# Kernel optimization log

Hardware: AMD Instinct MI355X
Metric: run time of the kernel (lower is better)

Reference implementation:

```python
import jax, jax.numpy as jnp
import numpy as np

SCORE_THRESH = 0.25
NMS_THRESH = 0.45
DETECTIONS = 100   # self.detections
K_CAND = 300       # fixed pre-NMS candidate count (jit-friendly stand-in for torch.where filtering)
STRIDES = (8, 16, 32)


def setup_inputs() -> dict:
    key = jax.random.key(0)
    ks = jax.random.split(key, 5)
    pred_p3 = jax.random.normal(ks[0], (16, 80, 80, 3, 85), jnp.float32)
    pred_p4 = jax.random.normal(ks[1], (16, 40, 40, 3, 85), jnp.float32)
    pred_p5 = jax.random.normal(ks[2], (16, 20, 20, 3, 85), jnp.float32)
    anchors = jnp.array([[[10, 13], [16, 30], [33, 23]],
                         [[30, 61], [62, 45], [59, 119]],
                         [[116, 90], [156, 198], [373, 326]]], jnp.float32)
    image_shapes = jnp.full((16, 2), 640, jnp.int32)  # (h, w) per image
    scale_factors = jax.random.uniform(ks[3], (16,), jnp.float32, 0.5, 1.5)
    return {"pred_p3": pred_p3, "pred_p4": pred_p4, "pred_p5": pred_p5,
            "anchors": anchors, "image_shapes": image_shapes,
            "scale_factors": scale_factors, "max_size": 4096}


def _decode_level(p, stride, anchor_wh):
    # p: [B,H,W,A,5+C] already sigmoided
    B, H, W, A, _ = p.shape
    gx = jnp.arange(W, dtype=p.dtype)
    gy = jnp.arange(H, dtype=p.dtype)
    grid = jnp.stack(jnp.meshgrid(gx, gy, indexing='xy'), axis=-1)  # [H,W,2] = (x,y)
    xy = (2.0 * p[..., :2] - 0.5 + grid[None, :, :, None, :]) * stride
    wh = 4.0 * p[..., 2:4] ** 2 * anchor_wh  # anchor_wh: [A,2]
    box = jnp.concatenate([xy, wh], axis=-1).reshape(B, H * W * A, 4)
    obj = p[..., 4].reshape(B, H * W * A)
    cls = p[..., 5:].reshape(B, H * W * A, -1)
    return box, obj, cls


def _pairwise_iou(b):  # b: [K,4] xyxy
    area = (b[:, 2] - b[:, 0]) * (b[:, 3] - b[:, 1])
    lt = jnp.maximum(b[:, None, :2], b[None, :, :2])
    rb = jnp.minimum(b[:, None, 2:], b[None, :, 2:])
    wh = jnp.clip(rb - lt, 0.0)
    inter = wh[..., 0] * wh[..., 1]
    return inter / (area[:, None] + area[None, :] - inter + 1e-9)


def _nms_image(boxes, scores, labels, im_shape, scale, max_size):
    # boxes [K,4], scores [K] sorted desc, labels [K] int
    w = im_shape[1].astype(boxes.dtype)
    h = im_shape[0].astype(boxes.dtype)
    boxes = jnp.stack([jnp.clip(boxes[:, 0], 0.0, w), jnp.clip(boxes[:, 1], 0.0, h),
                       jnp.clip(boxes[:, 2], 0.0, w), jnp.clip(boxes[:, 3], 0.0, h)], axis=1)
    # class-offset boxes (batched_nms)
    bn = jax.lax.stop_gradient(boxes + (labels.astype(boxes.dtype) * max_size)[:, None])
    iou = _pairwise_iou(bn)
    s_ng = jax.lax.stop_gradient(scores)
    K = boxes.shape[0]
    ar = jnp.arange(K)

    def body(i, keep):
        active = keep[i] & (s_ng[i] > SCORE_THRESH)
        return keep & ~((iou[i] > NMS_THRESH) & (ar > i) & active)

    keep = jax.lax.fori_loop(0, K, body, jnp.ones(K, bool))
    final = jnp.where(keep & (s_ng > SCORE_THRESH), scores, 0.0)
    det_s, det_i = jax.lax.top_k(final, DETECTIONS)
    det_b = boxes[det_i] / scale
    det_l = labels[det_i].astype(boxes.dtype)
    return jnp.concatenate([det_b, det_s[:, None], det_l[:, None]], axis=1)  # [D,6]


def reference(pred_p3, pred_p4, pred_p5, anchors, image_shapes, scale_factors, max_size):
    boxes_l, obj_l, cls_l = [], [], []
    for i, (pred, stride) in enumerate(zip((pred_p3, pred_p4, pred_p5), STRIDES)):
        p = jax.nn.sigmoid(pred)
        b, o, c = _decode_level(p, float(stride), anchors[i])
        boxes_l.append(b); obj_l.append(o); cls_l.append(c)
    boxes = jnp.concatenate(boxes_l, axis=1)   # [B,N,4] cxcywh
    obj = jnp.concatenate(obj_l, axis=1)       # [B,N]
    cls = jnp.concatenate(cls_l, axis=1)       # [B,N,C]
    # cxcywh -> xyxy
    cx, cy, ww, hh = boxes[..., 0], boxes[..., 1], boxes[..., 2], boxes[..., 3]
    boxes = jnp.stack([cx - ww / 2, cy - hh / 2, cx + ww / 2, cy + hh / 2], axis=-1)
    B, N, C = cls.shape
    logits = obj[..., None] * cls              # [B,N,C]
    valid = (obj[..., None] > SCORE_THRESH) & (logits > SCORE_THRESH)
    flat = jnp.where(valid, logits, 0.0).reshape(B, N * C)
    vals, idx = jax.lax.top_k(flat, K_CAND)    # sorted desc per image
    aidx = idx // C
    labels = idx % C
    cand_boxes = jnp.take_along_axis(boxes, aidx[..., None], axis=1)  # [B,K,4]
    out = jax.vmap(_nms_image, in_axes=(0, 0, 0, 0, 0, None))(
        cand_boxes, vals, labels, image_shapes, scale_factors, jnp.float32(max_size))
    return out  # [B, DETECTIONS, 6] = (x1,y1,x2,y2,score,label)
```

## Files before the change

kernel.cpp:

```cpp
#include <hip/hip_runtime.h>
#include <cstdint>
#include <cstddef>

#define BATCH 16
#define NCLS 80
#define NANCH 25200
#define ABINS 512
#define SBINS 1024
#define SCAP 2048
#define SCAP2 4096
#define LCAP 1024
#define KC 300
#define DET 100
#define SCORE_T 0.25f
#define NMS_T 0.45f
#define NBLK 50
#define SPAN 504
#define CNTPAD 16

#define TILES_PER_IMG 1575
#define TOT_TILES (BATCH * TILES_PER_IMG)
#define KMAX_BLOCKS 1575

__device__ __forceinline__ float sg(float x) { return 1.0f / (1.0f + expf(-x)); }

__device__ __forceinline__ const float* anchor_base(const float* p3, const float* p4,
                                                    const float* p5, int b, int n) {
    if (n < 19200) return p3 + ((size_t)b * 19200 + n) * 85;
    if (n < 24000) return p4 + ((size_t)b * 4800 + (n - 19200)) * 85;
    return p5 + ((size_t)b * 1200 + (n - 24000)) * 85;
}

__global__ __launch_bounds__(256) void k_max(const float* __restrict__ p3,
                                             const float* __restrict__ p4,
                                             const float* __restrict__ p5,
                                             float* __restrict__ gmax,
                                             unsigned int* __restrict__ ahist) {
    __shared__ __align__(16) float4 wbuf[4][340];
    int tid = threadIdx.x;
    int lane = tid & 63, wv = tid >> 6;
    float4* slot = wbuf[wv];
    const float* sf = (const float*)slot;
    int wid = blockIdx.x * 4 + wv;
    int g = lane >> 2, r = lane & 3;

    for (int t = wid; t < TOT_TILES; t += KMAX_BLOCKS * 4) {
        int b = t / TILES_PER_IMG, lt = t % TILES_PER_IMG;
        const float* src; int gidx;
        if (lt < 1200)      { src = p3 + ((size_t)b * 19200 + lt * 16) * 85;          gidx = lt * 16; }
        else if (lt < 1500) { src = p4 + ((size_t)b * 4800 + (lt - 1200) * 16) * 85;  gidx = 19200 + (lt - 1200) * 16; }
        else                { src = p5 + ((size_t)b * 1200 + (lt - 1500) * 16) * 85;  gidx = 24000 + (lt - 1500) * 16; }
        const float4* tp = (const float4*)src;

        float4 v0 = tp[lane];
        float4 v1 = tp[lane + 64];
        float4 v2 = tp[lane + 128];
        float4 v3 = tp[lane + 192];
        float4 v4 = tp[lane + 256];
        float4 v5 = make_float4(0.f, 0.f, 0.f, 0.f);
        bool ex = lane < 20;
        if (ex) v5 = tp[lane + 320];
        slot[lane] = v0;
        slot[lane + 64] = v1;
        slot[lane + 128] = v2;
        slot[lane + 192] = v3;
        slot[lane + 256] = v4;
        if (ex) slot[lane + 320] = v5;

        const float* cb = sf + 85 * g + 5 + 20 * r;
        float m = cb[0];
#pragma unroll
        for (int k = 1; k < 20; k++) m = fmaxf(m, cb[k]);
        m = fmaxf(m, __shfl_xor(m, 1, 64));
        m = fmaxf(m, __shfl_xor(m, 2, 64));

        if (r == 0) {
            float obj = sg(sf[85 * g + 4]);
            float v = 0.0f;
            if (obj > SCORE_T) v = obj * sg(m);
            gmax[(size_t)b * NANCH + gidx + g] = v;
            if (v > SCORE_T) {
                int bin = (int)((v - SCORE_T) * (ABINS / 0.75f));
                bin = bin < 0 ? 0 : (bin > ABINS - 1 ? ABINS - 1 : bin);
                atomicAdd(&ahist[b * ABINS + bin], 1u);
            }
        }
    }
}

__global__ __launch_bounds__(512) void k_collect(
    const float* __restrict__ p3, const float* __restrict__ p4, const float* __restrict__ p5,
    const float* __restrict__ gmax, const unsigned int* __restrict__ ahist,
    unsigned int* __restrict__ shist, unsigned int* __restrict__ scnt,
    float* __restrict__ ss, unsigned int* __restrict__ sidx) {
    __shared__ unsigned int h[ABINS];
    __shared__ unsigned int wtot[8], wsuf[8];
    __shared__ int TaS;
    __shared__ int an[SPAN];
    __shared__ float og[SPAN];
    __shared__ float lss[LCAP];
    __shared__ unsigned int lsi[LCAP];
    __shared__ unsigned int ncand, lcnt, gbase;
    int tid = threadIdx.x;
    int lane = tid & 63, wv = tid >> 6;
    int b = blockIdx.x / NBLK;
    int blk = blockIdx.x % NBLK;
    if (tid == 0) { ncand = 0u; TaS = 0; lcnt = 0u; }

    unsigned int run = ahist[b * ABINS + tid];
#pragma unroll
    for (int off = 1; off < 64; off <<= 1) {
        unsigned int v = __shfl_down(run, off, 64);
        if (lane + off < 64) run += v;
    }
    if (lane == 0) wtot[wv] = run;
    __syncthreads();
    if (wv == 0) {
        unsigned int r = (lane < 8) ? wtot[lane] : 0u;
#pragma unroll
        for (int off = 1; off < 8; off <<= 1) {
            unsigned int v = __shfl_down(r, off, 64);
            if (lane + off < 8) r += v;
        }
        if (lane < 8) wsuf[lane] = r;
    }
    __syncthreads();
    unsigned int suf = run + ((wv < 7) ? wsuf[wv + 1] : 0u);
    h[tid] = suf;
    __syncthreads();
    if (suf >= KC && (tid == ABINS - 1 || h[tid + 1] < KC)) TaS = tid;
    __syncthreads();
    int Ta = TaS;

    int n0 = blk * SPAN;
    for (int i = tid; i < SPAN; i += 512) {
        int n = n0 + i;
        float v = gmax[(size_t)b * NANCH + n];
        if (v > SCORE_T) {
            int bin = (int)((v - SCORE_T) * (ABINS / 0.75f));
            bin = bin < 0 ? 0 : (bin > ABINS - 1 ? ABINS - 1 : bin);
            if (bin >= Ta) {
                unsigned int p = atomicAdd(&ncand, 1u);
                an[p] = n;
            }
        }
    }
    __syncthreads();
    int M = (int)ncand;
    for (int i = tid; i < M; i += 512) {
        const float* pb = anchor_base(p3, p4, p5, b, an[i]);
        og[i] = sg(pb[4]);
    }
    __syncthreads();
    int twoTa = 2 * Ta;
    for (int idx = tid; idx < M * NCLS; idx += 512) {
        int a = idx / NCLS, c = idx - a * NCLS;
        const float* pb = anchor_base(p3, p4, p5, b, an[a]);
        float s = og[a] * sg(pb[5 + c]);
        if (s > SCORE_T) {
            int bin = (int)((s - SCORE_T) * (SBINS / 0.75f));
            bin = bin < 0 ? 0 : (bin > SBINS - 1 ? SBINS - 1 : bin);
            if (bin >= twoTa) {
                atomicAdd(&shist[b * SBINS + bin], 1u);
                unsigned int p = atomicAdd(&lcnt, 1u);
                if (p < LCAP) {
                    lss[p] = s;
                    lsi[p] = (unsigned int)(an[a] * NCLS + c);
                } else {
                    unsigned int q = atomicAdd(&scnt[b * CNTPAD], 1u);
                    if (q < SCAP2) {
                        ss[(size_t)b * SCAP2 + q] = s;
                        sidx[(size_t)b * SCAP2 + q] = (unsigned int)(an[a] * NCLS + c);
                    }
                }
            }
        }
    }
    __syncthreads();
    unsigned int nl = lcnt < LCAP ? lcnt : LCAP;
    if (tid == 0 && nl > 0) gbase = atomicAdd(&scnt[b * CNTPAD], nl);
    __syncthreads();
    for (unsigned int i = tid; i < nl; i += 512) {
        unsigned int p = gbase + i;
        if (p < SCAP2) {
            ss[(size_t)b * SCAP2 + p] = lss[i];
            sidx[(size_t)b * SCAP2 + p] = lsi[i];
        }
    }
}

struct NmsBuf {
    unsigned long long msk[KC * 5];
    float4 bx[KC];
    int lab[KC];
    float sc2[KC];
    float ar[KC];
    unsigned long long keep[5];
    unsigned int actw[10];
    int wpref[6];
    int order[DET];
    int okept[DET];
};

__global__ __launch_bounds__(1024) void k_img(
    const float* __restrict__ p3, const float* __restrict__ p4, const float* __restrict__ p5,
    const float* __restrict__ anchors, const int* __restrict__ imshapes,
    const float* __restrict__ scalef,
    const unsigned int* __restrict__ shist, const unsigned int* __restrict__ scnt_g,
    const float* __restrict__ ss, const unsigned int* __restrict__ sidx,
    float* __restrict__ out) {
    __shared__ unsigned int hist[SBINS];
    __shared__ __align__(16) NmsBuf u;
    __shared__ float cs[SCAP];
    __shared__ unsigned int ci[SCAP];
    __shared__ float sv[KC];
    __shared__ unsigned int si[KC];
    __shared__ unsigned int wtot[16], wsuf[16];
    __shared__ unsigned int scnt_s;
    __shared__ int TsS;

    int b = blockIdx.x;
    int tid = threadIdx.x;
    int lane = tid & 63, wv = tid >> 6;
    if (tid == 0) { scnt_s = 0u; TsS = 0; }

    unsigned int run = shist[b * SBINS + tid];
#pragma unroll
    for (int off = 1; off < 64; off <<= 1) {
        unsigned int v = __shfl_down(run, off, 64);
        if (lane + off < 64) run += v;
    }
    if (lane == 0) wtot[wv] = run;
    __syncthreads();
    if (wv == 0) {
        unsigned int r = (lane < 16) ? wtot[lane] : 0u;
#pragma unroll
        for (int off = 1; off < 16; off <<= 1) {
            unsigned int v = __shfl_down(r, off, 64);
            if (lane + off < 16) r += v;
        }
        if (lane < 16) wsuf[lane] = r;
    }
    __syncthreads();
    unsigned int suf = run + ((wv < 15) ? wsuf[wv + 1] : 0u);
    hist[tid] = suf;
    __syncthreads();
    if (suf >= KC && (tid == SBINS - 1 || hist[tid + 1] < KC)) TsS = tid;
    __syncthreads();
    int Ts = TsS;

    unsigned int total = scnt_g[b * CNTPAD];
    int navail = (int)(total < SCAP2 ? total : SCAP2);
    for (int i = tid; i < navail; i += 1024) {
        float s = ss[(size_t)b * SCAP2 + i];
        int bin = (int)((s - SCORE_T) * (SBINS / 0.75f));
        bin = bin < 0 ? 0 : (bin > SBINS - 1 ? SBINS - 1 : bin);
        if (bin >= Ts) {
            unsigned int pos = atomicAdd(&scnt_s, 1u);
            if (pos < SCAP) { cs[pos] = s; ci[pos] = sidx[(size_t)b * SCAP2 + i]; }
        }
    }
    __syncthreads();
    int nc = (int)(scnt_s < SCAP ? scnt_s : SCAP);

    if (tid < KC) { sv[tid] = 0.f; si[tid] = 0xffffffffu; }
    __syncthreads();
    for (int i = tid; i < nc; i += 1024) {
        float s = cs[i];
        unsigned int ii = ci[i];
        int r = 0;
        for (int j = 0; j < nc; j++) {
            float sj = cs[j];
            unsigned int ij = ci[j];
            if (sj > s || (sj == s && ij < ii)) r++;
        }
        if (r < KC) { sv[r] = s; si[r] = ii; }
    }
    __syncthreads();
    int valid = nc < KC ? nc : KC;

    if (tid < KC) {
        int i = tid;
        if (i < valid) {
            unsigned int fi = si[i];
            int n = (int)(fi / NCLS), c = (int)(fi % NCLS);
            int lvl = (n < 19200) ? 0 : (n < 24000 ? 1 : 2);
            const int offl[3] = {0, 19200, 24000};
            const int Wl[3] = {80, 40, 20};
            const int cntl[3] = {19200, 4800, 1200};
            const float strl[3] = {8.f, 16.f, 32.f};
            const float* pp = lvl == 0 ? p3 : (lvl == 1 ? p4 : p5);
            int nl = n - offl[lvl];
            int a = nl % 3, cell = nl / 3;
            int gx = cell % Wl[lvl], gy = cell / Wl[lvl];
            const float* pb = pp + ((size_t)b * cntl[lvl] + nl) * 85;
            float s0 = sg(pb[0]), s1 = sg(pb[1]), s2 = sg(pb[2]), s3 = sg(pb[3]);
            float stride = strl[lvl];
            float aw = anchors[(lvl * 3 + a) * 2 + 0];
            float ah = anchors[(lvl * 3 + a) * 2 + 1];
            float cx = (2.0f * s0 - 0.5f + (float)gx) * stride;
            float cy = (2.0f * s1 - 0.5f + (float)gy) * stride;
            float bw = 4.0f * s2 * s2 * aw;
            float bh = 4.0f * s3 * s3 * ah;
            float hf = (float)imshapes[b * 2 + 0];
            float wf = (float)imshapes[b * 2 + 1];
            float x1 = cx - bw / 2.0f, y1 = cy - bh / 2.0f;
            float x2 = cx + bw / 2.0f, y2 = cy + bh / 2.0f;
            x1 = fminf(fmaxf(x1, 0.f), wf);
            y1 = fminf(fmaxf(y1, 0.f), hf);
            x2 = fminf(fmaxf(x2, 0.f), wf);
            y2 = fminf(fmaxf(y2, 0.f), hf);
            u.bx[i] = make_float4(x1, y1, x2, y2);
            u.lab[i] = c;
            u.sc2[i] = sv[i];
            u.ar[i] = (x2 - x1) * (y2 - y1);
        } else {
            u.bx[i] = make_float4(0, 0, 0, 0);
            u.lab[i] = -1 - i;
            u.sc2[i] = 0.f;
            u.ar[i] = 0.f;
        }
    }
    __syncthreads();

    if (tid < 10) u.actw[tid] = 0u;
    for (int t = tid; t < KC * 5; t += 1024) {
        int i = t / 5, w = t % 5;
        float4 bi = u.bx[i];
        int li = u.lab[i];
        float ai = u.ar[i];
        unsigned long long m = 0ull;
        for (int tb = 0; tb < 64; tb++) {
            int j = w * 64 + tb;
            if (j < KC && j > i && u.lab[j] == li) {
                float4 bj = u.bx[j];
                float ltx = fmaxf(bi.x, bj.x), lty = fmaxf(bi.y, bj.y);
                float rbx = fminf(bi.z, bj.z), rby = fminf(bi.w, bj.w);
                float iw = fmaxf(rbx - ltx, 0.f), ih = fmaxf(rby - lty, 0.f);
                float inter = iw * ih;
                float iou = inter / (ai + u.ar[j] - inter + 1e-9f);
                if (iou > NMS_T) m |= (1ull << tb);
            }
        }
        u.msk[t] = m;
    }
    __syncthreads();

    for (int i = tid; i < KC; i += 1024) {
        unsigned long long nz = u.msk[i * 5] | u.msk[i * 5 + 1] | u.msk[i * 5 + 2] |
                                u.msk[i * 5 + 3] | u.msk[i * 5 + 4];
        if (nz) atomicOr(&u.actw[i >> 5], 1u << (i & 31));
    }
    __syncthreads();
    if (tid == 0) {
        u.keep[0] = u.keep[1] = u.keep[2] = u.keep[3] = u.keep[4] = ~0ull;
        for (int w = 0; w < 10; w++) {
            unsigned int mw = u.actw[w];
            while (mw) {
                int bpos = __ffs(mw) - 1;
                mw &= mw - 1;
                int i = w * 32 + bpos;
                if ((u.keep[i >> 6] >> (i & 63)) & 1ull) {
#pragma unroll
                    for (int r = 0; r < 5; r++) u.keep[r] &= ~u.msk[i * 5 + r];
                }
            }
        }
        int s = 0;
        for (int w = 0; w < 5; w++) {
            unsigned long long kw = u.keep[w];
            if (w == 4) kw &= (1ull << 44) - 1ull;
            u.wpref[w] = s;
            s += (int)__popcll(kw);
        }
        u.wpref[5] = s;
    }
    __syncthreads();

    if (tid < KC) {
        int w = tid >> 6, bp = tid & 63;
        unsigned long long kw = u.keep[w];
        bool kept = (kw >> bp) & 1ull;
        int r = u.wpref[w] + (int)__popcll(kw & ((1ull << bp) - 1ull));
        if (kept) {
            if (r < DET) { u.order[r] = tid; u.okept[r] = 1; }
        } else {
            int nr = u.wpref[5] + (tid - r);
            if (nr < DET) { u.order[nr] = tid; u.okept[nr] = 0; }
        }
    }
    __syncthreads();

    if (tid < DET) {
        int o = u.order[tid];
        float scale = scalef[b];
        float4 bb = u.bx[o];
        float s = (u.okept[tid] && o < valid) ? u.sc2[o] : 0.f;
        float lb = (o < valid) ? (float)u.lab[o] : 0.f;
        float* po = out + ((size_t)b * DET + tid) * 6;
        po[0] = bb.x / scale;
        po[1] = bb.y / scale;
        po[2] = bb.z / scale;
        po[3] = bb.w / scale;
        po[4] = s;
        po[5] = lb;
    }
}

extern "C" void kernel_launch(void* const* d_in, const int* in_sizes, int n_in,
                              void* d_out, int out_size, void* d_ws, size_t ws_size,
                              hipStream_t stream) {
    const float* p3 = (const float*)d_in[0];
    const float* p4 = (const float*)d_in[1];
    const float* p5 = (const float*)d_in[2];
    const float* anchors = (const float*)d_in[3];
    const int* imshapes = (const int*)d_in[4];
    const float* scalef = (const float*)d_in[5];
    float* out = (float*)d_out;

    char* ws = (char*)d_ws;
    float* gmax = (float*)ws;
    unsigned int* ahist = (unsigned int*)(ws + 1612800);
    unsigned int* shist = (unsigned int*)(ws + 1612800 + 32768);
    unsigned int* scnt  = (unsigned int*)(ws + 1612800 + 32768 + 65536);
    float* ss           = (float*)(ws + 1612800 + 32768 + 65536 + 1024);
    unsigned int* sidx  = (unsigned int*)(ws + 1612800 + 32768 + 65536 + 1024 + 262144);

    hipMemsetAsync(ws + 1612800, 0, 32768 + 65536 + 1024, stream);

    k_max<<<KMAX_BLOCKS, 256, 0, stream>>>(p3, p4, p5, gmax, ahist);
    k_collect<<<BATCH * NBLK, 512, 0, stream>>>(p3, p4, p5, gmax, ahist, shist, scnt, ss, sidx);
    k_img<<<BATCH, 1024, 0, stream>>>(p3, p4, p5, anchors, imshapes, scalef,
                                      shist, scnt, ss, sidx, out);
}
```

Baseline: 234.7 us.

## Precompute box decode in collect stage and prefetch candidate scores in NMS kernel

Box decoding (sigmoid of the box terms, grid and anchor math) moves from the single-block-per-image NMS kernel into the wide collect kernel. The decoded cx,cy,w,h for each surviving candidate is stored in a new workspace array, and the NMS kernel looks it up through a short position index. The NMS kernel also issues its score and index loads before the histogram scan and finds the threshold bin with a shuffle instead of a shared-memory pass. The class-max loop in k_max now reads with an interleaved stride, which changes the LDS access pattern. The cost is extra decode work and global writes for every collected candidate, not only the top 300.

```diff
diff --git a/kernel.cpp b/kernel.cpp
--- a/kernel.cpp
+++ b/kernel.cpp
@@ -67,10 +67,10 @@
         slot[lane + 256] = v4;
         if (ex) slot[lane + 320] = v5;
 
-        const float* cb = sf + 85 * g + 5 + 20 * r;
+        const float* cb = sf + 85 * g + 5 + r;
         float m = cb[0];
 #pragma unroll
-        for (int k = 1; k < 20; k++) m = fmaxf(m, cb[k]);
+        for (int k = 1; k < 20; k++) m = fmaxf(m, cb[4 * k]);
         m = fmaxf(m, __shfl_xor(m, 1, 64));
         m = fmaxf(m, __shfl_xor(m, 2, 64));
 
@@ -90,9 +90,10 @@
 
 __global__ __launch_bounds__(512) void k_collect(
     const float* __restrict__ p3, const float* __restrict__ p4, const float* __restrict__ p5,
+    const float* __restrict__ anchors,
     const float* __restrict__ gmax, const unsigned int* __restrict__ ahist,
     unsigned int* __restrict__ shist, unsigned int* __restrict__ scnt,
-    float* __restrict__ ss, unsigned int* __restrict__ sidx) {
+    float* __restrict__ ss, unsigned int* __restrict__ sidx, float4* __restrict__ dec) {
     __shared__ unsigned int h[ABINS];
     __shared__ unsigned int wtot[8], wsuf[8];
     __shared__ int TaS;
@@ -100,6 +101,7 @@
     __shared__ float og[SPAN];
     __shared__ float lss[LCAP];
     __shared__ unsigned int lsi[LCAP];
+    __shared__ __align__(16) float4 ldec[LCAP];
     __shared__ unsigned int ncand, lcnt, gbase;
     int tid = threadIdx.x;
     int lane = tid & 63, wv = tid >> 6;
@@ -155,22 +157,42 @@
     int twoTa = 2 * Ta;
     for (int idx = tid; idx < M * NCLS; idx += 512) {
         int a = idx / NCLS, c = idx - a * NCLS;
-        const float* pb = anchor_base(p3, p4, p5, b, an[a]);
+        int n = an[a];
+        const float* pb = anchor_base(p3, p4, p5, b, n);
         float s = og[a] * sg(pb[5 + c]);
         if (s > SCORE_T) {
             int bin = (int)((s - SCORE_T) * (SBINS / 0.75f));
             bin = bin < 0 ? 0 : (bin > SBINS - 1 ? SBINS - 1 : bin);
             if (bin >= twoTa) {
+                int lvl = (n < 19200) ? 0 : (n < 24000 ? 1 : 2);
+                const int offl[3] = {0, 19200, 24000};
+                const int Wl[3] = {80, 40, 20};
+                const float strl[3] = {8.f, 16.f, 32.f};
+                int nl = n - offl[lvl];
+                int aa = nl % 3, cell = nl / 3;
+                int gx = cell % Wl[lvl], gy = cell / Wl[lvl];
+                float s0 = sg(pb[0]), s1 = sg(pb[1]), s2 = sg(pb[2]), s3 = sg(pb[3]);
+                float stride = strl[lvl];
+                float aw = anchors[(lvl * 3 + aa) * 2 + 0];
+                float ah = anchors[(lvl * 3 + aa) * 2 + 1];
+                float cx = (2.0f * s0 - 0.5f + (float)gx) * stride;
+                float cy = (2.0f * s1 - 0.5f + (float)gy) * stride;
+                float bw = 4.0f * s2 * s2 * aw;
+                float bh = 4.0f * s3 * s3 * ah;
+                float4 d4 = make_float4(cx, cy, bw, bh);
+
                 atomicAdd(&shist[b * SBINS + bin], 1u);
                 unsigned int p = atomicAdd(&lcnt, 1u);
                 if (p < LCAP) {
                     lss[p] = s;
-                    lsi[p] = (unsigned int)(an[a] * NCLS + c);
+                    lsi[p] = (unsigned int)(n * NCLS + c);
+                    ldec[p] = d4;
                 } else {
                     unsigned int q = atomicAdd(&scnt[b * CNTPAD], 1u);
                     if (q < SCAP2) {
                         ss[(size_t)b * SCAP2 + q] = s;
-                        sidx[(size_t)b * SCAP2 + q] = (unsigned int)(an[a] * NCLS + c);
+                        sidx[(size_t)b * SCAP2 + q] = (unsigned int)(n * NCLS + c);
+                        dec[(size_t)b * SCAP2 + q] = d4;
                     }
                 }
             }
@@ -185,6 +207,7 @@
         if (p < SCAP2) {
             ss[(size_t)b * SCAP2 + p] = lss[i];
             sidx[(size_t)b * SCAP2 + p] = lsi[i];
+            dec[(size_t)b * SCAP2 + p] = ldec[i];
         }
     }
 }
@@ -203,18 +226,17 @@
 };
 
 __global__ __launch_bounds__(1024) void k_img(
-    const float* __restrict__ p3, const float* __restrict__ p4, const float* __restrict__ p5,
-    const float* __restrict__ anchors, const int* __restrict__ imshapes,
-    const float* __restrict__ scalef,
+    const int* __restrict__ imshapes, const float* __restrict__ scalef,
     const unsigned int* __restrict__ shist, const unsigned int* __restrict__ scnt_g,
     const float* __restrict__ ss, const unsigned int* __restrict__ sidx,
-    float* __restrict__ out) {
-    __shared__ unsigned int hist[SBINS];
+    const float4* __restrict__ dec, float* __restrict__ out) {
     __shared__ __align__(16) NmsBuf u;
     __shared__ float cs[SCAP];
     __shared__ unsigned int ci[SCAP];
+    __shared__ unsigned short cp[SCAP];
     __shared__ float sv[KC];
     __shared__ unsigned int si[KC];
+    __shared__ unsigned short sp[KC];
     __shared__ unsigned int wtot[16], wsuf[16];
     __shared__ unsigned int scnt_s;
     __shared__ int TsS;
@@ -224,6 +246,16 @@
     int lane = tid & 63, wv = tid >> 6;
     if (tid == 0) { scnt_s = 0u; TsS = 0; }
 
+    unsigned int total = scnt_g[b * CNTPAD];
+    float ps0 = ss[(size_t)b * SCAP2 + tid];
+    float ps1 = ss[(size_t)b * SCAP2 + tid + 1024];
+    float ps2 = ss[(size_t)b * SCAP2 + tid + 2048];
+    float ps3 = ss[(size_t)b * SCAP2 + tid + 3072];
+    unsigned int pi0 = sidx[(size_t)b * SCAP2 + tid];
+    unsigned int pi1 = sidx[(size_t)b * SCAP2 + tid + 1024];
+    unsigned int pi2 = sidx[(size_t)b * SCAP2 + tid + 2048];
+    unsigned int pi3 = sidx[(size_t)b * SCAP2 + tid + 3072];
+
     unsigned int run = shist[b * SBINS + tid];
 #pragma unroll
     for (int off = 1; off < 64; off <<= 1) {
@@ -242,28 +274,33 @@
         if (lane < 16) wsuf[lane] = r;
     }
     __syncthreads();
-    unsigned int suf = run + ((wv < 15) ? wsuf[wv + 1] : 0u);
-    hist[tid] = suf;
-    __syncthreads();
-    if (suf >= KC && (tid == SBINS - 1 || hist[tid + 1] < KC)) TsS = tid;
+    unsigned int tail = (wv < 15) ? wsuf[wv + 1] : 0u;
+    unsigned int suf = run + tail;
+    unsigned int sufn = __shfl_down(suf, 1, 64);
+    if (lane == 63) sufn = tail;
+    if (suf >= KC && (tid == SBINS - 1 || sufn < KC)) TsS = tid;
     __syncthreads();
     int Ts = TsS;
 
-    unsigned int total = scnt_g[b * CNTPAD];
     int navail = (int)(total < SCAP2 ? total : SCAP2);
-    for (int i = tid; i < navail; i += 1024) {
-        float s = ss[(size_t)b * SCAP2 + i];
-        int bin = (int)((s - SCORE_T) * (SBINS / 0.75f));
-        bin = bin < 0 ? 0 : (bin > SBINS - 1 ? SBINS - 1 : bin);
-        if (bin >= Ts) {
-            unsigned int pos = atomicAdd(&scnt_s, 1u);
-            if (pos < SCAP) { cs[pos] = s; ci[pos] = sidx[(size_t)b * SCAP2 + i]; }
+#pragma unroll
+    for (int k = 0; k < 4; k++) {
+        int i = tid + k * 1024;
+        float s = k == 0 ? ps0 : (k == 1 ? ps1 : (k == 2 ? ps2 : ps3));
+        unsigned int fi = k == 0 ? pi0 : (k == 1 ? pi1 : (k == 2 ? pi2 : pi3));
+        if (i < navail) {
+            int bin = (int)((s - SCORE_T) * (SBINS / 0.75f));
+            bin = bin < 0 ? 0 : (bin > SBINS - 1 ? SBINS - 1 : bin);
+            if (bin >= Ts) {
+                unsigned int pos = atomicAdd(&scnt_s, 1u);
+                if (pos < SCAP) { cs[pos] = s; ci[pos] = fi; cp[pos] = (unsigned short)i; }
+            }
         }
     }
     __syncthreads();
     int nc = (int)(scnt_s < SCAP ? scnt_s : SCAP);
 
-    if (tid < KC) { sv[tid] = 0.f; si[tid] = 0xffffffffu; }
+    if (tid < KC) { sv[tid] = 0.f; si[tid] = 0xffffffffu; sp[tid] = 0; }
     __syncthreads();
     for (int i = tid; i < nc; i += 1024) {
         float s = cs[i];
@@ -274,7 +311,7 @@
             unsigned int ij = ci[j];
             if (sj > s || (sj == s && ij < ii)) r++;
         }
-        if (r < KC) { sv[r] = s; si[r] = ii; }
+        if (r < KC) { sv[r] = s; si[r] = ii; sp[r] = cp[i]; }
     }
     __syncthreads();
     int valid = nc < KC ? nc : KC;
@@ -282,30 +319,12 @@
     if (tid < KC) {
         int i = tid;
         if (i < valid) {
-            unsigned int fi = si[i];
-            int n = (int)(fi / NCLS), c = (int)(fi % NCLS);
-            int lvl = (n < 19200) ? 0 : (n < 24000 ? 1 : 2);
-            const int offl[3] = {0, 19200, 24000};
-            const int Wl[3] = {80, 40, 20};
-            const int cntl[3] = {19200, 4800, 1200};
-            const float strl[3] = {8.f, 16.f, 32.f};
-            const float* pp = lvl == 0 ? p3 : (lvl == 1 ? p4 : p5);
-            int nl = n - offl[lvl];
-            int a = nl % 3, cell = nl / 3;
-            int gx = cell % Wl[lvl], gy = cell / Wl[lvl];
-            const float* pb = pp + ((size_t)b * cntl[lvl] + nl) * 85;
-            float s0 = sg(pb[0]), s1 = sg(pb[1]), s2 = sg(pb[2]), s3 = sg(pb[3]);
-            float stride = strl[lvl];
-            float aw = anchors[(lvl * 3 + a) * 2 + 0];
-            float ah = anchors[(lvl * 3 + a) * 2 + 1];
-            float cx = (2.0f * s0 - 0.5f + (float)gx) * stride;
-            float cy = (2.0f * s1 - 0.5f + (float)gy) * stride;
-            float bw = 4.0f * s2 * s2 * aw;
-            float bh = 4.0f * s3 * s3 * ah;
+            float4 d = dec[(size_t)b * SCAP2 + sp[i]];
+            int c = (int)(si[i] % NCLS);
             float hf = (float)imshapes[b * 2 + 0];
             float wf = (float)imshapes[b * 2 + 1];
-            float x1 = cx - bw / 2.0f, y1 = cy - bh / 2.0f;
-            float x2 = cx + bw / 2.0f, y2 = cy + bh / 2.0f;
+            float x1 = d.x - d.z / 2.0f, y1 = d.y - d.w / 2.0f;
+            float x2 = d.x + d.z / 2.0f, y2 = d.y + d.w / 2.0f;
             x1 = fminf(fmaxf(x1, 0.f), wf);
             y1 = fminf(fmaxf(y1, 0.f), hf);
             x2 = fminf(fmaxf(x2, 0.f), wf);
@@ -425,11 +444,12 @@
     unsigned int* scnt  = (unsigned int*)(ws + 1612800 + 32768 + 65536);
     float* ss           = (float*)(ws + 1612800 + 32768 + 65536 + 1024);
     unsigned int* sidx  = (unsigned int*)(ws + 1612800 + 32768 + 65536 + 1024 + 262144);
+    float4* dec         = (float4*)(ws + 1612800 + 32768 + 65536 + 1024 + 262144 + 262144);
 
     hipMemsetAsync(ws + 1612800, 0, 32768 + 65536 + 1024, stream);
 
     k_max<<<KMAX_BLOCKS, 256, 0, stream>>>(p3, p4, p5, gmax, ahist);
-    k_collect<<<BATCH * NBLK, 512, 0, stream>>>(p3, p4, p5, gmax, ahist, shist, scnt, ss, sidx);
-    k_img<<<BATCH, 1024, 0, stream>>>(p3, p4, p5, anchors, imshapes, scalef,
-                                      shist, scnt, ss, sidx, out);
+    k_collect<<<BATCH * NBLK, 512, 0, stream>>>(p3, p4, p5, anchors, gmax, ahist,
+                                                shist, scnt, ss, sidx, dec);
+    k_img<<<BATCH, 1024, 0, stream>>>(imshapes, scalef, shist, scnt, ss, sidx, dec, out);
 }
```

New measurement: 233.4 us. Within noise of the previous version (-0.6%).

## Fold candidate collection into per-image NMS kernel, dropping score histogram pass

Applied to the files above, without the earlier changes.

Removes the separate k_collect launch and its global score histogram and staging buffers. Each per-image block now scans all anchors' gmax values against the anchor-histogram threshold, then expands survivors to per-class scores directly into shared memory before ranking. This saves one launch, the global atomics and a memset. In exchange the collection work runs on only 16 blocks instead of 800, and candidates are filtered only by the coarser anchor-based threshold, so the quadratic rank sort may see more entries.

```diff
diff --git a/kernel.cpp b/kernel.cpp
--- a/kernel.cpp
+++ b/kernel.cpp
@@ -7,16 +7,12 @@
 #define NANCH 25200
 #define ABINS 512
 #define SBINS 1024
+#define ACAP 2048
 #define SCAP 2048
-#define SCAP2 4096
-#define LCAP 1024
 #define KC 300
 #define DET 100
 #define SCORE_T 0.25f
 #define NMS_T 0.45f
-#define NBLK 50
-#define SPAN 504
-#define CNTPAD 16
 
 #define TILES_PER_IMG 1575
 #define TOT_TILES (BATCH * TILES_PER_IMG)
@@ -88,107 +84,6 @@
     }
 }
 
-__global__ __launch_bounds__(512) void k_collect(
-    const float* __restrict__ p3, const float* __restrict__ p4, const float* __restrict__ p5,
-    const float* __restrict__ gmax, const unsigned int* __restrict__ ahist,
-    unsigned int* __restrict__ shist, unsigned int* __restrict__ scnt,
-    float* __restrict__ ss, unsigned int* __restrict__ sidx) {
-    __shared__ unsigned int h[ABINS];
-    __shared__ unsigned int wtot[8], wsuf[8];
-    __shared__ int TaS;
-    __shared__ int an[SPAN];
-    __shared__ float og[SPAN];
-    __shared__ float lss[LCAP];
-    __shared__ unsigned int lsi[LCAP];
-    __shared__ unsigned int ncand, lcnt, gbase;
-    int tid = threadIdx.x;
-    int lane = tid & 63, wv = tid >> 6;
-    int b = blockIdx.x / NBLK;
-    int blk = blockIdx.x % NBLK;
-    if (tid == 0) { ncand = 0u; TaS = 0; lcnt = 0u; }
-
-    unsigned int run = ahist[b * ABINS + tid];
-#pragma unroll
-    for (int off = 1; off < 64; off <<= 1) {
-        unsigned int v = __shfl_down(run, off, 64);
-        if (lane + off < 64) run += v;
-    }
-    if (lane == 0) wtot[wv] = run;
-    __syncthreads();
-    if (wv == 0) {
-        unsigned int r = (lane < 8) ? wtot[lane] : 0u;
-#pragma unroll
-        for (int off = 1; off < 8; off <<= 1) {
-            unsigned int v = __shfl_down(r, off, 64);
-            if (lane + off < 8) r += v;
-        }
-        if (lane < 8) wsuf[lane] = r;
-    }
-    __syncthreads();
-    unsigned int suf = run + ((wv < 7) ? wsuf[wv + 1] : 0u);
-    h[tid] = suf;
-    __syncthreads();
-    if (suf >= KC && (tid == ABINS - 1 || h[tid + 1] < KC)) TaS = tid;
-    __syncthreads();
-    int Ta = TaS;
-
-    int n0 = blk * SPAN;
-    for (int i = tid; i < SPAN; i += 512) {
-        int n = n0 + i;
-        float v = gmax[(size_t)b * NANCH + n];
-        if (v > SCORE_T) {
-            int bin = (int)((v - SCORE_T) * (ABINS / 0.75f));
-            bin = bin < 0 ? 0 : (bin > ABINS - 1 ? ABINS - 1 : bin);
-            if (bin >= Ta) {
-                unsigned int p = atomicAdd(&ncand, 1u);
-                an[p] = n;
-            }
-        }
-    }
-    __syncthreads();
-    int M = (int)ncand;
-    for (int i = tid; i < M; i += 512) {
-        const float* pb = anchor_base(p3, p4, p5, b, an[i]);
-        og[i] = sg(pb[4]);
-    }
-    __syncthreads();
-    int twoTa = 2 * Ta;
-    for (int idx = tid; idx < M * NCLS; idx += 512) {
-        int a = idx / NCLS, c = idx - a * NCLS;
-        const float* pb = anchor_base(p3, p4, p5, b, an[a]);
-        float s = og[a] * sg(pb[5 + c]);
-        if (s > SCORE_T) {
-            int bin = (int)((s - SCORE_T) * (SBINS / 0.75f));
-            bin = bin < 0 ? 0 : (bin > SBINS - 1 ? SBINS - 1 : bin);
-            if (bin >= twoTa) {
-                atomicAdd(&shist[b * SBINS + bin], 1u);
-                unsigned int p = atomicAdd(&lcnt, 1u);
-                if (p < LCAP) {
-                    lss[p] = s;
-                    lsi[p] = (unsigned int)(an[a] * NCLS + c);
-                } else {
-                    unsigned int q = atomicAdd(&scnt[b * CNTPAD], 1u);
-                    if (q < SCAP2) {
-                        ss[(size_t)b * SCAP2 + q] = s;
-                        sidx[(size_t)b * SCAP2 + q] = (unsigned int)(an[a] * NCLS + c);
-                    }
-                }
-            }
-        }
-    }
-    __syncthreads();
-    unsigned int nl = lcnt < LCAP ? lcnt : LCAP;
-    if (tid == 0 && nl > 0) gbase = atomicAdd(&scnt[b * CNTPAD], nl);
-    __syncthreads();
-    for (unsigned int i = tid; i < nl; i += 512) {
-        unsigned int p = gbase + i;
-        if (p < SCAP2) {
-            ss[(size_t)b * SCAP2 + p] = lss[i];
-            sidx[(size_t)b * SCAP2 + p] = lsi[i];
-        }
-    }
-}
-
 struct NmsBuf {
     unsigned long long msk[KC * 5];
     float4 bx[KC];
@@ -205,71 +100,93 @@
 __global__ __launch_bounds__(1024) void k_img(
     const float* __restrict__ p3, const float* __restrict__ p4, const float* __restrict__ p5,
     const float* __restrict__ anchors, const int* __restrict__ imshapes,
-    const float* __restrict__ scalef,
-    const unsigned int* __restrict__ shist, const unsigned int* __restrict__ scnt_g,
-    const float* __restrict__ ss, const unsigned int* __restrict__ sidx,
-    float* __restrict__ out) {
-    __shared__ unsigned int hist[SBINS];
+    const float* __restrict__ scalef, const float* __restrict__ gmax,
+    const unsigned int* __restrict__ ahist, float* __restrict__ out) {
     __shared__ __align__(16) NmsBuf u;
     __shared__ float cs[SCAP];
     __shared__ unsigned int ci[SCAP];
+    __shared__ unsigned short alist[ACAP];
     __shared__ float sv[KC];
     __shared__ unsigned int si[KC];
-    __shared__ unsigned int wtot[16], wsuf[16];
-    __shared__ unsigned int scnt_s;
-    __shared__ int TsS;
+    __shared__ unsigned int wtot[8], wsuf[8];
+    __shared__ unsigned int ncand, lcnt;
+    __shared__ int TaS;
 
     int b = blockIdx.x;
     int tid = threadIdx.x;
     int lane = tid & 63, wv = tid >> 6;
-    if (tid == 0) { scnt_s = 0u; TsS = 0; }
-
-    unsigned int run = shist[b * SBINS + tid];
+    if (tid == 0) { ncand = 0u; lcnt = 0u; TaS = 0; }
+    __syncthreads();
+
+    unsigned int run = 0;
+    if (tid < ABINS) run = ahist[b * ABINS + tid];
 #pragma unroll
     for (int off = 1; off < 64; off <<= 1) {
         unsigned int v = __shfl_down(run, off, 64);
         if (lane + off < 64) run += v;
     }
-    if (lane == 0) wtot[wv] = run;
+    if (lane == 0 && wv < 8) wtot[wv] = run;
     __syncthreads();
     if (wv == 0) {
-        unsigned int r = (lane < 16) ? wtot[lane] : 0u;
+        unsigned int r = (lane < 8) ? wtot[lane] : 0u;
 #pragma unroll
-        for (int off = 1; off < 16; off <<= 1) {
+        for (int off = 1; off < 8; off <<= 1) {
             unsigned int v = __shfl_down(r, off, 64);
-            if (lane + off < 16) r += v;
-        }
-        if (lane < 16) wsuf[lane] = r;
-    }
-    __syncthreads();
-    unsigned int suf = run + ((wv < 15) ? wsuf[wv + 1] : 0u);
-    hist[tid] = suf;
-    __syncthreads();
-    if (suf >= KC && (tid == SBINS - 1 || hist[tid + 1] < KC)) TsS = tid;
-    __syncthreads();
-    int Ts = TsS;
-
-    unsigned int total = scnt_g[b * CNTPAD];
-    int navail = (int)(total < SCAP2 ? total : SCAP2);
-    for (int i = tid; i < navail; i += 1024) {
-        float s = ss[(size_t)b * SCAP2 + i];
-        int bin = (int)((s - SCORE_T) * (SBINS / 0.75f));
-        bin = bin < 0 ? 0 : (bin > SBINS - 1 ? SBINS - 1 : bin);
-        if (bin >= Ts) {
-            unsigned int pos = atomicAdd(&scnt_s, 1u);
-            if (pos < SCAP) { cs[pos] = s; ci[pos] = sidx[(size_t)b * SCAP2 + i]; }
-        }
-    }
-    __syncthreads();
-    int nc = (int)(scnt_s < SCAP ? scnt_s : SCAP);
+            if (lane + off < 8) r += v;
+        }
+        if (lane < 8) wsuf[lane] = r;
+    }
+    __syncthreads();
+    if (tid < ABINS) {
+        unsigned int tail = (wv < 7) ? wsuf[wv + 1] : 0u;
+        unsigned int suf = run + tail;
+        unsigned int sufn = __shfl_down(suf, 1, 64);
+        if (lane == 63) sufn = tail;
+        if (suf >= KC && (tid == ABINS - 1 || sufn < KC)) TaS = tid;
+    }
+    __syncthreads();
+    int Ta = TaS;
+
+    for (int n = tid; n < NANCH; n += 1024) {
+        float v = gmax[(size_t)b * NANCH + n];
+        if (v > SCORE_T) {
+            int bin = (int)((v - SCORE_T) * (ABINS / 0.75f));
+            bin = bin < 0 ? 0 : (bin > ABINS - 1 ? ABINS - 1 : bin);
+            if (bin >= Ta) {
+                unsigned int p = atomicAdd(&ncand, 1u);
+                if (p < ACAP) alist[p] = (unsigned short)n;
+            }
+        }
+    }
+    __syncthreads();
+    int M = (int)(ncand < ACAP ? ncand : ACAP);
+    int twoTa = 2 * Ta;
+
+    for (int idx = tid; idx < M * NCLS; idx += 1024) {
+        int a = idx / NCLS, c = idx - a * NCLS;
+        int n = (int)alist[a];
+        const float* pb = anchor_base(p3, p4, p5, b, n);
+        float obj = sg(pb[4]);
+        float s = obj * sg(pb[5 + c]);
+        if (s > SCORE_T) {
+            int bin = (int)((s - SCORE_T) * (SBINS / 0.75f));
+            bin = bin < 0 ? 0 : (bin > SBINS - 1 ? SBINS - 1 : bin);
+            if (bin >= twoTa) {
+                unsigned int p = atomicAdd(&lcnt, 1u);
+                if (p < SCAP) { cs[p] = s; ci[p] = (unsigned int)(n * NCLS + c); }
+            }
+        }
+    }
+    __syncthreads();
+    int nl = (int)(lcnt < SCAP ? lcnt : SCAP);
 
     if (tid < KC) { sv[tid] = 0.f; si[tid] = 0xffffffffu; }
     __syncthreads();
-    for (int i = tid; i < nc; i += 1024) {
+    for (int i = tid; i < nl; i += 1024) {
         float s = cs[i];
         unsigned int ii = ci[i];
         int r = 0;
-        for (int j = 0; j < nc; j++) {
+        for (int j = 0; j < nl; j++) {
             float sj = cs[j];
             unsigned int ij = ci[j];
             if (sj > s || (sj == s && ij < ii)) r++;
@@ -277,7 +194,7 @@
         if (r < KC) { sv[r] = s; si[r] = ii; }
     }
     __syncthreads();
-    int valid = nc < KC ? nc : KC;
+    int valid = nl < KC ? nl : KC;
 
     if (tid < KC) {
         int i = tid;
@@ -290,10 +207,10 @@
             const int cntl[3] = {19200, 4800, 1200};
             const float strl[3] = {8.f, 16.f, 32.f};
             const float* pp = lvl == 0 ? p3 : (lvl == 1 ? p4 : p5);
-            int nl = n - offl[lvl];
-            int a = nl % 3, cell = nl / 3;
+            int nn = n - offl[lvl];
+            int a = nn % 3, cell = nn / 3;
             int gx = cell % Wl[lvl], gy = cell / Wl[lvl];
-            const float* pb = pp + ((size_t)b * cntl[lvl] + nl) * 85;
+            const float* pb = pp + ((size_t)b * cntl[lvl] + nn) * 85;
             float s0 = sg(pb[0]), s1 = sg(pb[1]), s2 = sg(pb[2]), s3 = sg(pb[3]);
             float stride = strl[lvl];
             float aw = anchors[(lvl * 3 + a) * 2 + 0];
@@ -421,15 +338,10 @@
     char* ws = (char*)d_ws;
     float* gmax = (float*)ws;
     unsigned int* ahist = (unsigned int*)(ws + 1612800);
-    unsigned int* shist = (unsigned int*)(ws + 1612800 + 32768);
-    unsigned int* scnt  = (unsigned int*)(ws + 1612800 + 32768 + 65536);
-    float* ss           = (float*)(ws + 1612800 + 32768 + 65536 + 1024);
-    unsigned int* sidx  = (unsigned int*)(ws + 1612800 + 32768 + 65536 + 1024 + 262144);
-
-    hipMemsetAsync(ws + 1612800, 0, 32768 + 65536 + 1024, stream);
+
+    hipMemsetAsync(ws + 1612800, 0, 32768, stream);
 
     k_max<<<KMAX_BLOCKS, 256, 0, stream>>>(p3, p4, p5, gmax, ahist);
-    k_collect<<<BATCH * NBLK, 512, 0, stream>>>(p3, p4, p5, gmax, ahist, shist, scnt, ss, sidx);
     k_img<<<BATCH, 1024, 0, stream>>>(p3, p4, p5, anchors, imshapes, scalef,
-                                      shist, scnt, ss, sidx, out);
+                                      gmax, ahist, out);
 }
```

New measurement: 261.2 us. 1.11x slower.
